# Performance work log

Measured on AMD Instinct MI355X. Metric: run time of the kernel, lower is better.

Reference implementation:

```python
import jax, jax.numpy as jnp
import numpy as np

B, T, D = 8, 8192, 768
H, HD = 12, 64            # heads, head_dim
Q_STRIDE = 4              # flattened 2x2 q pooling
WINDOW = 64               # flattened mask-unit size after pooling
SCALE = HD ** -0.5


def setup_inputs() -> dict:
    key = jax.random.key(0)
    ks = jax.random.split(key, 5)
    return {
        "embeddings": jax.random.normal(ks[0], (B, T, D), jnp.float32),
        "qkv_w": jax.random.normal(ks[1], (3 * D, D), jnp.float32) * 0.02,
        "qkv_b": jax.random.normal(ks[2], (3 * D,), jnp.float32) * 0.02,
        "proj_w": jax.random.normal(ks[3], (D, D), jnp.float32) * 0.02,
        "proj_b": jax.random.normal(ks[4], (D,), jnp.float32) * 0.02,
    }


def reference(embeddings, qkv_w, qkv_b, proj_w, proj_b):
    b, t, _ = embeddings.shape
    nw = t // (Q_STRIDE * WINDOW)          # number of mask-unit windows
    seq = t // nw                           # tokens per window (pre q-pool)
    # qkv: [b, t, 3D] -> [b, seq, nw, 3, H, HD] (windows are interleaved along tokens)
    qkv = (embeddings @ qkv_w.T + qkv_b).reshape(b, seq, nw, 3, H, HD)
    qkv = jnp.transpose(qkv, (3, 0, 4, 2, 1, 5))  # [3, b, H, nw, seq, HD]
    q, k, v = qkv[0], qkv[1], qkv[2]
    # q max-pool over stride groups (interleaved split of seq)
    q = q.reshape(b, H, nw, Q_STRIDE, seq // Q_STRIDE, HD).max(axis=3)
    attn = jax.nn.softmax(
        jnp.einsum("bhwqd,bhwkd->bhwqk", q * SCALE, k), axis=-1
    )  # [b, H, nw, q_len, seq]
    out = jnp.einsum("bhwqk,bhwkd->bhwqd", attn, v)  # [b, H, nw, q_len, HD]
    out = jnp.transpose(out, (0, 3, 2, 1, 4)).reshape(b, -1, H * HD)
    out = out @ proj_w.T + proj_b
    return out, attn
```

## Files before the change

kernel.cpp:

```cpp
#include <hip/hip_runtime.h>
#include <hip/hip_bf16.h>


typedef float  f32x4  __attribute__((ext_vector_type(4)));
typedef __bf16 bf16x8 __attribute__((ext_vector_type(8)));

__device__ __forceinline__ unsigned short f2bf(float f) {
  unsigned int u = __float_as_uint(f);
  u += 0x7fffu + ((u >> 16) & 1u);
  return (unsigned short)(u >> 16);
}
__device__ __forceinline__ float bf2f(unsigned short b) {
  return __uint_as_float(((unsigned int)b) << 16);
}

#define GLOAD_LDS16(gptr, lptr) __builtin_amdgcn_global_load_lds( \
    (const __attribute__((address_space(1))) void*)(gptr),        \
    (__attribute__((address_space(3))) void*)(lptr), 16, 0, 0)

__global__ void cvt_bf16(const float* __restrict__ src,
                         unsigned short* __restrict__ dst, int n4) {
  int i = blockIdx.x * blockDim.x + threadIdx.x;
  const int stride = gridDim.x * blockDim.x;
  for (; i < n4; i += stride) {
    const float4 v = ((const float4*)src)[i];
    ushort4 o;
    o.x = f2bf(v.x); o.y = f2bf(v.y); o.z = f2bf(v.z); o.w = f2bf(v.w);
    ((ushort4*)dst)[i] = o;
  }
}

template <int OUT_BF16>
__global__ __launch_bounds__(512, 2) void gemm256p(
    const unsigned short* __restrict__ A, const unsigned short* __restrict__ B,
    const float* __restrict__ bias, void* __restrict__ Cout,
    int M, int N, int K) {
  extern __shared__ char lds[];

  const int tid  = threadIdx.x;
  const int lane = tid & 63;
  const int wid  = tid >> 6;
  const int g16  = (lane >> 4) & 3;
  const int l15  = lane & 15;
  const int wm   = wid >> 2;
  const int wn   = wid & 3;

  const size_t bm = (size_t)blockIdx.x << 8;
  const int NT = K >> 6;
  const int NB = N >> 8;
  const int TT = NB * NT;

  const int srow = tid >> 2;
  const int csel = (((tid & 3) ^ ((tid >> 3) & 3)) << 3);
  const int ldst = wid * 1024;
  const unsigned short* pA0 = A + (bm + srow) * (size_t)K + csel;
  const unsigned short* pA1 = pA0 + (size_t)128 * K;
  const unsigned short* pB0 = B + (size_t)srow * K + csel;
  const unsigned short* pB1 = pB0 + (size_t)128 * K;

#define STAGE_A(koff, regbase)                                          \
  do {                                                                  \
    GLOAD_LDS16(pA0 + (koff), lds + (regbase) + ldst);                  \
    GLOAD_LDS16(pA1 + (koff), lds + (regbase) + 8192 + ldst);           \
  } while (0)
#define STAGE_B(boff, regbase)                                          \
  do {                                                                  \
    GLOAD_LDS16(pB0 + (boff), lds + (regbase) + ldst);                  \
    GLOAD_LDS16(pB1 + (boff), lds + (regbase) + 8192 + ldst);           \
  } while (0)

  const int s16  = ((g16 ^ ((l15 >> 1) & 3)) << 4);
  const int offA = (wm * 128 + l15) * 64 + s16;
  const int offB = (wn * 64 + l15) * 64 + s16;

  f32x4 acc[8][4];
  const f32x4 zero4 = {0.f, 0.f, 0.f, 0.f};
#pragma unroll
  for (int i = 0; i < 8; ++i)
#pragma unroll
    for (int j = 0; j < 4; ++j) acc[i][j] = zero4;

#define READ_A(par, kk, rh)                                              \
  { const char* rb = lds + (par) * 32768 + (kk) * 16384 + offA + (rh) * 4096; \
    af[0] = *(const bf16x8*)(rb);                                        \
    af[1] = *(const bf16x8*)(rb + 1024);                                 \
    af[2] = *(const bf16x8*)(rb + 2048);                                 \
    af[3] = *(const bf16x8*)(rb + 3072); }
#define READ_B(par, kk)                                                  \
  { const char* rb = lds + 65536 + (par) * 32768 + (kk) * 16384 + offB;  \
    bfv[0] = *(const bf16x8*)(rb);                                       \
    bfv[1] = *(const bf16x8*)(rb + 1024);                                \
    bfv[2] = *(const bf16x8*)(rb + 2048);                                \
    bfv[3] = *(const bf16x8*)(rb + 3072); }
#define MFMA16(rh)                                                       \
  _Pragma("unroll") for (int q = 0; q < 4; ++q)                          \
  _Pragma("unroll") for (int c = 0; c < 4; ++c)                          \
    acc[(rh) * 4 + q][c] = __builtin_amdgcn_mfma_f32_16x16x32_bf16(      \
        af[q], bfv[c], acc[(rh) * 4 + q][c], 0, 0, 0);
#define BAR() __builtin_amdgcn_s_barrier()
#define VMCNT8() asm volatile("s_waitcnt vmcnt(8)" ::: "memory")

  int    kk  = 0;
  int    bnC = 0;
  int    k1  = 64;
  int    k2  = 128;
  size_t rB1 = 0;
  size_t rB2 = 0;

  STAGE_A(0, 0);
  STAGE_B(0, 65536);
  STAGE_A(32, 16384);
  STAGE_B(32, 65536 + 16384);
  STAGE_A(64, 32768);
  STAGE_B(64, 65536 + 32768);
  VMCNT8();
  BAR();

  for (int s = 0; s < TT; ++s) {
    const int par  = s & 1;
    const int parn = par ^ 1;
    bf16x8 af[4], bfv[4];

    READ_A(par, 0, 0); READ_B(par, 0);
    STAGE_A(k1 + 32, parn * 32768 + 16384);
    BAR();
    __builtin_amdgcn_s_setprio(1); MFMA16(0); __builtin_amdgcn_s_setprio(0);
    BAR();

    READ_A(par, 0, 1);
    STAGE_B(rB1 + k1 + 32, 65536 + parn * 32768 + 16384);
    VMCNT8();
    BAR();
    __builtin_amdgcn_s_setprio(1); MFMA16(1); __builtin_amdgcn_s_setprio(0);
    BAR();

    READ_A(par, 1, 0); READ_B(par, 1);
    STAGE_A(k2, par * 32768);
    BAR();
    __builtin_amdgcn_s_setprio(1); MFMA16(0); __builtin_amdgcn_s_setprio(0);
    BAR();

    READ_A(par, 1, 1);
    STAGE_B(rB2 + k2, 65536 + par * 32768);
    VMCNT8();
    BAR();
    __builtin_amdgcn_s_setprio(1); MFMA16(1); __builtin_amdgcn_s_setprio(0);
    BAR();

    if (kk == NT - 1) {
#pragma unroll
      for (int ai = 0; ai < 8; ++ai) {
        const size_t row0 =
            bm + wm * 128 + (ai >> 2) * 64 + (ai & 3) * 16 + g16 * 4;
#pragma unroll
        for (int c = 0; c < 4; ++c) {
          const int col = bnC + wn * 64 + c * 16 + l15;
          const float bv = bias[col];
#pragma unroll
          for (int r = 0; r < 4; ++r) {
            const float v = acc[ai][c][r] + bv;
            const size_t idx = (row0 + r) * (size_t)N + col;
            if (OUT_BF16) ((unsigned short*)Cout)[idx] = f2bf(v);
            else          ((float*)Cout)[idx] = v;
          }
          acc[ai][c] = zero4;
        }
      }
      bnC += 256;
      kk = 0;
    } else {
      ++kk;
    }

    k1 = k2; rB1 = rB2;
    if (s + 3 < TT) {
      k2 += 64;
      if (k2 == K) { k2 = 0; rB2 += (size_t)256 * K; }
    }
  }
#undef STAGE_A
#undef STAGE_B
#undef READ_A
#undef READ_B
#undef MFMA16
#undef BAR
#undef VMCNT8
}

template <int OUT_BF16>
__global__ __launch_bounds__(256) void gemm_bt(
    const unsigned short* __restrict__ A, const unsigned short* __restrict__ B,
    const float* __restrict__ bias, void* __restrict__ Cout,
    int M, int N, int K) {
  __shared__ unsigned short As[128 * 64];
  __shared__ unsigned short Bs[128 * 64];

  const int tid  = threadIdx.x;
  const int lane = tid & 63;
  const int wid  = tid >> 6;
  const int g16  = lane >> 4;
  const int l15  = lane & 15;
  const int bm = blockIdx.x * 128;
  const int bn = blockIdx.y * 128;
  const int wr = (wid >> 1) * 64;
  const int wc = (wid & 1) * 64;

  const f32x4 zero4 = {0.f, 0.f, 0.f, 0.f};
  f32x4 acc[4][4];
#pragma unroll
  for (int m = 0; m < 4; ++m)
#pragma unroll
    for (int n = 0; n < 4; ++n) acc[m][n] = zero4;

  const int flatBase = tid * 16;

  for (int kt = 0; kt < K; kt += 64) {
#pragma unroll
    for (int c = 0; c < 4; ++c) {
      const int flat = c * 4096 + flatBase;
      const int row  = flat >> 7;
      const int cole = (flat & 127) >> 1;
      const unsigned short* ga = A + (size_t)(bm + row) * K + kt + cole;
      const unsigned short* gb = B + (size_t)(bn + row) * K + kt + cole;
      GLOAD_LDS16(ga, (char*)As + c * 4096 + wid * 1024);
      GLOAD_LDS16(gb, (char*)Bs + c * 4096 + wid * 1024);
    }
    __syncthreads();
#pragma unroll
    for (int kk = 0; kk < 2; ++kk) {
      bf16x8 af[4], bfv[4];
#pragma unroll
      for (int m = 0; m < 4; ++m)
        af[m] = *(const bf16x8*)((const char*)As +
                 ((wr + m * 16 + l15) * 64 + kk * 32 + g16 * 8) * 2);
#pragma unroll
      for (int n = 0; n < 4; ++n)
        bfv[n] = *(const bf16x8*)((const char*)Bs +
                 ((wc + n * 16 + l15) * 64 + kk * 32 + g16 * 8) * 2);
#pragma unroll
      for (int m = 0; m < 4; ++m)
#pragma unroll
        for (int n = 0; n < 4; ++n)
          acc[m][n] = __builtin_amdgcn_mfma_f32_16x16x32_bf16(af[m], bfv[n],
                                                              acc[m][n], 0, 0, 0);
    }
    __syncthreads();
  }

#pragma unroll
  for (int n = 0; n < 4; ++n) {
    const int col = bn + wc + n * 16 + l15;
    const float bv = bias[col];
#pragma unroll
    for (int m = 0; m < 4; ++m) {
      const int rowb = bm + wr + m * 16 + g16 * 4;
#pragma unroll
      for (int r = 0; r < 4; ++r) {
        const float v = acc[m][n][r] + bv;
        const size_t idx = (size_t)(rowb + r) * N + col;
        if (OUT_BF16) ((unsigned short*)Cout)[idx] = f2bf(v);
        else          ((float*)Cout)[idx] = v;
      }
    }
  }
}

__global__ __launch_bounds__(256) void attn_kernel(
    const unsigned short* __restrict__ qkv,
    float* __restrict__ attn_out,
    unsigned short* __restrict__ Xws) {
  __shared__ unsigned short smem[32768];
  char* KP = (char*)smem;
  char* VT = (char*)(smem + 16384);

  const int tid  = threadIdx.x;
  const int lane = tid & 63;
  const int wid  = tid >> 6;
  const int g16  = lane >> 4;
  const int l15  = lane & 15;

  const int bid = blockIdx.x;
  const int w = bid & 31;
  const int h = (bid >> 5) % 12;
  const int b = bid / 384;

  {
    const int s0 = tid >> 3;
    const int part = tid & 7;
#pragma unroll
    for (int p = 0; p < 8; ++p) {
      const int s = s0 + p * 32;
      const size_t gbase =
          ((size_t)b * 8192 + (size_t)s * 32 + w) * 2304 + h * 64 + part * 8;
      int4 kv = *(const int4*)(qkv + gbase + 768);
      *(int4*)(KP + ((s * 128 + part * 16) ^ ((s & 7) << 4))) = kv;
      int4 vv = *(const int4*)(qkv + gbase + 1536);
      const unsigned short* pv = (const unsigned short*)&vv;
#pragma unroll
      for (int j = 0; j < 8; ++j) {
        const int d = part * 8 + j;
        *(unsigned short*)(VT + ((d * 512 + s * 2) ^ ((d & 7) << 4))) = pv[j];
      }
    }
  }

  union BU { unsigned short u[8]; bf16x8 v; };
  BU aq0, aq1;
  {
    const int qrow = wid * 16 + l15;
    float q0[8], q1[8];
#pragma unroll
    for (int j = 0; j < 8; ++j) { q0[j] = -1e30f; q1[j] = -1e30f; }
#pragma unroll
    for (int g = 0; g < 4; ++g) {
      const size_t gbase =
          ((size_t)b * 8192 + (size_t)(g * 64 + qrow) * 32 + w) * 2304 +
          h * 64 + g16 * 8;
      int4 a = *(const int4*)(qkv + gbase);
      int4 c = *(const int4*)(qkv + gbase + 32);
      const unsigned short* pa = (const unsigned short*)&a;
      const unsigned short* pc = (const unsigned short*)&c;
#pragma unroll
      for (int j = 0; j < 8; ++j) {
        q0[j] = fmaxf(q0[j], bf2f(pa[j]));
        q1[j] = fmaxf(q1[j], bf2f(pc[j]));
      }
    }
#pragma unroll
    for (int j = 0; j < 8; ++j) {
      aq0.u[j] = (unsigned short)(__float_as_uint(q0[j]) >> 16);
      aq1.u[j] = (unsigned short)(__float_as_uint(q1[j]) >> 16);
    }
  }

  __syncthreads();

  f32x4 sacc[16];
  const f32x4 zero4 = {0.f, 0.f, 0.f, 0.f};
#pragma unroll
  for (int t = 0; t < 16; ++t) sacc[t] = zero4;
#pragma unroll
  for (int t = 0; t < 16; ++t) {
    const int srow = t * 16 + l15;
    bf16x8 bk0 = *(const bf16x8*)(KP + ((srow * 128 + 0  + g16 * 16) ^ ((srow & 7) << 4)));
    bf16x8 bk1 = *(const bf16x8*)(KP + ((srow * 128 + 64 + g16 * 16) ^ ((srow & 7) << 4)));
    sacc[t] = __builtin_amdgcn_mfma_f32_16x16x32_bf16(aq0.v, bk0, sacc[t], 0, 0, 0);
    sacc[t] = __builtin_amdgcn_mfma_f32_16x16x32_bf16(aq1.v, bk1, sacc[t], 0, 0, 0);
  }

  float inv_[4];
#pragma unroll
  for (int r = 0; r < 4; ++r) {
    float m = -1e30f;
#pragma unroll
    for (int t = 0; t < 16; ++t) { sacc[t][r] *= 0.125f; m = fmaxf(m, sacc[t][r]); }
#pragma unroll
    for (int off = 1; off < 16; off <<= 1) m = fmaxf(m, __shfl_xor(m, off, 64));
    float ssum = 0.f;
#pragma unroll
    for (int t = 0; t < 16; ++t) {
      float e = expf(sacc[t][r] - m);
      sacc[t][r] = e;
      ssum += e;
    }
#pragma unroll
    for (int off = 1; off < 16; off <<= 1) ssum += __shfl_xor(ssum, off, 64);
    inv_[r] = 1.f / ssum;
  }

  {
    float* ab = attn_out + ((size_t)bid * 64 + wid * 16) * 256;
#pragma unroll
    for (int t = 0; t < 16; ++t)
#pragma unroll
      for (int r = 0; r < 4; ++r) {
        const float p = sacc[t][r] * inv_[r];
        sacc[t][r] = p;
        ab[(size_t)(g16 * 4 + r) * 256 + t * 16 + l15] = p;
      }
  }

  __syncthreads();

  {
    char* PW = KP + wid * 8192;
#pragma unroll
    for (int t = 0; t < 16; ++t)
#pragma unroll
      for (int r = 0; r < 4; ++r) {
        const int row = g16 * 4 + r;
        *(unsigned short*)(PW + ((row * 512 + (t * 16 + l15) * 2) ^ ((row & 7) << 4))) =
            f2bf(sacc[t][r]);
      }
  }

  f32x4 oacc[4];
#pragma unroll
  for (int n = 0; n < 4; ++n) oacc[n] = zero4;
  {
    const char* PR = KP + wid * 8192;
#pragma unroll
    for (int kc = 0; kc < 8; ++kc) {
      bf16x8 pa = *(const bf16x8*)(PR + ((l15 * 512 + kc * 64 + g16 * 16) ^ ((l15 & 7) << 4)));
#pragma unroll
      for (int n = 0; n < 4; ++n) {
        const int d = n * 16 + l15;
        bf16x8 vv = *(const bf16x8*)(VT + ((d * 512 + kc * 64 + g16 * 16) ^ ((d & 7) << 4)));
        oacc[n] = __builtin_amdgcn_mfma_f32_16x16x32_bf16(pa, vv, oacc[n], 0, 0, 0);
      }
    }
  }

#pragma unroll
  for (int n = 0; n < 4; ++n)
#pragma unroll
    for (int r = 0; r < 4; ++r) {
      const int qi = wid * 16 + g16 * 4 + r;
      Xws[((size_t)b * 2048 + qi * 32 + w) * 768 + h * 64 + n * 16 + l15] =
          f2bf(oacc[n][r]);
    }
}

extern "C" void kernel_launch(void* const* d_in, const int* in_sizes, int n_in,
                              void* d_out, int out_size, void* d_ws, size_t ws_size,
                              hipStream_t stream) {
  const float* emb    = (const float*)d_in[0];
  const float* qkv_w  = (const float*)d_in[1];
  const float* qkv_b  = (const float*)d_in[2];
  const float* proj_w = (const float*)d_in[3];
  const float* proj_b = (const float*)d_in[4];
  float* out = (float*)d_out;

  char* ws = (char*)d_ws;
  unsigned short* embB   = (unsigned short*)(ws);
  unsigned short* wqkvB  = (unsigned short*)(ws + 100663296);
  unsigned short* wprojB = (unsigned short*)(ws + 104202240);
  unsigned short* qkvB   = (unsigned short*)(ws + 105381888);
  unsigned short* Xws    = (unsigned short*)(ws + 407371776);

  cvt_bf16<<<4096, 256, 0, stream>>>(emb, embB, 50331648 / 4);
  cvt_bf16<<<1728, 256, 0, stream>>>(qkv_w, wqkvB, 1769472 / 4);
  cvt_bf16<<<576, 256, 0, stream>>>(proj_w, wprojB, 589824 / 4);

  hipFuncSetAttribute(reinterpret_cast<const void*>(&gemm256p<1>),
                      hipFuncAttributeMaxDynamicSharedMemorySize, 131072);
  gemm256p<1><<<256, 512, 131072, stream>>>(embB, wqkvB, qkv_b, qkvB,
                                            65536, 2304, 768);

  attn_kernel<<<3072, 256, 0, stream>>>(qkvB, out + 12582912, Xws);

  gemm_bt<0><<<dim3(128, 6), 256, 0, stream>>>(Xws, wprojB, proj_b, out,
                                               16384, 768, 768);
}
```

Baseline: 489.5 us.

## Double-buffer LDS fragment registers to prefetch next MFMA operands

```diff
diff --git a/kernel.cpp b/kernel.cpp
--- a/kernel.cpp
+++ b/kernel.cpp
@@ -80,25 +80,27 @@
 #pragma unroll
     for (int j = 0; j < 4; ++j) acc[i][j] = zero4;
 
-#define READ_A(par, kk, rh)                                              \
+  bf16x8 aA[4], aB[4], bA[4], bB[4];
+
+#define READ_A_TO(dst, par, kk, rh)                                      \
   { const char* rb = lds + (par) * 32768 + (kk) * 16384 + offA + (rh) * 4096; \
-    af[0] = *(const bf16x8*)(rb);                                        \
-    af[1] = *(const bf16x8*)(rb + 1024);                                 \
-    af[2] = *(const bf16x8*)(rb + 2048);                                 \
-    af[3] = *(const bf16x8*)(rb + 3072); }
-#define READ_B(par, kk)                                                  \
+    dst[0] = *(const bf16x8*)(rb);                                       \
+    dst[1] = *(const bf16x8*)(rb + 1024);                                \
+    dst[2] = *(const bf16x8*)(rb + 2048);                                \
+    dst[3] = *(const bf16x8*)(rb + 3072); }
+#define READ_B_TO(dst, par, kk)                                          \
   { const char* rb = lds + 65536 + (par) * 32768 + (kk) * 16384 + offB;  \
-    bfv[0] = *(const bf16x8*)(rb);                                       \
-    bfv[1] = *(const bf16x8*)(rb + 1024);                                \
-    bfv[2] = *(const bf16x8*)(rb + 2048);                                \
-    bfv[3] = *(const bf16x8*)(rb + 3072); }
-#define MFMA16(rh)                                                       \
+    dst[0] = *(const bf16x8*)(rb);                                       \
+    dst[1] = *(const bf16x8*)(rb + 1024);                                \
+    dst[2] = *(const bf16x8*)(rb + 2048);                                \
+    dst[3] = *(const bf16x8*)(rb + 3072); }
+#define MFMA16(av, bv, rh)                                               \
   _Pragma("unroll") for (int q = 0; q < 4; ++q)                          \
   _Pragma("unroll") for (int c = 0; c < 4; ++c)                          \
     acc[(rh) * 4 + q][c] = __builtin_amdgcn_mfma_f32_16x16x32_bf16(      \
-        af[q], bfv[c], acc[(rh) * 4 + q][c], 0, 0, 0);
+        av[q], bv[c], acc[(rh) * 4 + q][c], 0, 0, 0);
 #define BAR() __builtin_amdgcn_s_barrier()
-#define VMCNT8() asm volatile("s_waitcnt vmcnt(8)" ::: "memory")
+#define VMCNT6() asm volatile("s_waitcnt vmcnt(6)" ::: "memory")
 
   int    kk  = 0;
   int    bnC = 0;
@@ -113,38 +115,41 @@
   STAGE_B(32, 65536 + 16384);
   STAGE_A(64, 32768);
   STAGE_B(64, 65536 + 32768);
-  VMCNT8();
+  asm volatile("s_waitcnt vmcnt(8)" ::: "memory");
   BAR();
+  READ_A_TO(aA, 0, 0, 0);
+  READ_B_TO(bA, 0, 0);
 
   for (int s = 0; s < TT; ++s) {
     const int par  = s & 1;
     const int parn = par ^ 1;
-    bf16x8 af[4], bfv[4];
-
-    READ_A(par, 0, 0); READ_B(par, 0);
+
+    READ_A_TO(aB, par, 0, 1);
     STAGE_A(k1 + 32, parn * 32768 + 16384);
-    BAR();
-    __builtin_amdgcn_s_setprio(1); MFMA16(0); __builtin_amdgcn_s_setprio(0);
-    BAR();
-
-    READ_A(par, 0, 1);
+    VMCNT6();
+    BAR();
+    __builtin_amdgcn_s_setprio(1); MFMA16(aA, bA, 0); __builtin_amdgcn_s_setprio(0);
+    BAR();
+
+    READ_A_TO(aA, par, 1, 0);
+    READ_B_TO(bB, par, 1);
     STAGE_B(rB1 + k1 + 32, 65536 + parn * 32768 + 16384);
-    VMCNT8();
-    BAR();
-    __builtin_amdgcn_s_setprio(1); MFMA16(1); __builtin_amdgcn_s_setprio(0);
-    BAR();
-
-    READ_A(par, 1, 0); READ_B(par, 1);
+    BAR();
+    __builtin_amdgcn_s_setprio(1); MFMA16(aB, bA, 1); __builtin_amdgcn_s_setprio(0);
+    BAR();
+
+    READ_A_TO(aB, par, 1, 1);
     STAGE_A(k2, par * 32768);
-    BAR();
-    __builtin_amdgcn_s_setprio(1); MFMA16(0); __builtin_amdgcn_s_setprio(0);
-    BAR();
-
-    READ_A(par, 1, 1);
+    VMCNT6();
+    BAR();
+    __builtin_amdgcn_s_setprio(1); MFMA16(aA, bB, 0); __builtin_amdgcn_s_setprio(0);
+    BAR();
+
+    READ_A_TO(aA, parn, 0, 0);
+    READ_B_TO(bA, parn, 0);
     STAGE_B(rB2 + k2, 65536 + par * 32768);
-    VMCNT8();
-    BAR();
-    __builtin_amdgcn_s_setprio(1); MFMA16(1); __builtin_amdgcn_s_setprio(0);
+    BAR();
+    __builtin_amdgcn_s_setprio(1); MFMA16(aB, bB, 1); __builtin_amdgcn_s_setprio(0);
     BAR();
 
     if (kk == NT - 1) {
@@ -180,11 +185,11 @@
   }
 #undef STAGE_A
 #undef STAGE_B
-#undef READ_A
-#undef READ_B
+#undef READ_A_TO
+#undef READ_B_TO
 #undef MFMA16
 #undef BAR
-#undef VMCNT8
+#undef VMCNT6
 }
 
 template <int OUT_BF16>
```

Result: no change. 487.5 us (-0.4%).

## Swizzle GEMM LDS tiles and vectorize V transpose stores in attention

Applied to the files above, without the earlier changes.

```diff
diff --git a/kernel.cpp b/kernel.cpp
--- a/kernel.cpp
+++ b/kernel.cpp
@@ -213,17 +213,19 @@
     for (int n = 0; n < 4; ++n) acc[m][n] = zero4;
 
   const int flatBase = tid * 16;
+  const int rsw = l15 & 3;
 
   for (int kt = 0; kt < K; kt += 64) {
 #pragma unroll
     for (int c = 0; c < 4; ++c) {
       const int flat = c * 4096 + flatBase;
       const int row  = flat >> 7;
-      const int cole = (flat & 127) >> 1;
+      const int slot = (flat >> 4) & 7;
+      const int cole = (((slot) ^ (row & 3)) << 3);
       const unsigned short* ga = A + (size_t)(bm + row) * K + kt + cole;
       const unsigned short* gb = B + (size_t)(bn + row) * K + kt + cole;
-      GLOAD_LDS16(ga, (char*)As + c * 4096 + wid * 1024);
-      GLOAD_LDS16(gb, (char*)Bs + c * 4096 + wid * 1024);
+      GLOAD_LDS16(ga, (char*)As + c * 4096 + wid * 1024 + lane * 16);
+      GLOAD_LDS16(gb, (char*)Bs + c * 4096 + wid * 1024 + lane * 16);
     }
     __syncthreads();
 #pragma unroll
@@ -232,11 +234,11 @@
 #pragma unroll
       for (int m = 0; m < 4; ++m)
         af[m] = *(const bf16x8*)((const char*)As +
-                 ((wr + m * 16 + l15) * 64 + kk * 32 + g16 * 8) * 2);
+                 (wr + m * 16 + l15) * 128 + (((kk * 4 + g16) ^ rsw) << 4));
 #pragma unroll
       for (int n = 0; n < 4; ++n)
         bfv[n] = *(const bf16x8*)((const char*)Bs +
-                 ((wc + n * 16 + l15) * 64 + kk * 32 + g16 * 8) * 2);
+                 (wc + n * 16 + l15) * 128 + (((kk * 4 + g16) ^ rsw) << 4));
 #pragma unroll
       for (int m = 0; m < 4; ++m)
 #pragma unroll
@@ -284,23 +286,43 @@
   const int h = (bid >> 5) % 12;
   const int b = bid / 384;
 
-  {
-    const int s0 = tid >> 3;
-    const int part = tid & 7;
-#pragma unroll
-    for (int p = 0; p < 8; ++p) {
-      const int s = s0 + p * 32;
-      const size_t gbase =
-          ((size_t)b * 8192 + (size_t)s * 32 + w) * 2304 + h * 64 + part * 8;
-      int4 kv = *(const int4*)(qkv + gbase + 768);
-      *(int4*)(KP + ((s * 128 + part * 16) ^ ((s & 7) << 4))) = kv;
-      int4 vv = *(const int4*)(qkv + gbase + 1536);
-      const unsigned short* pv = (const unsigned short*)&vv;
-#pragma unroll
-      for (int j = 0; j < 8; ++j) {
-        const int d = part * 8 + j;
-        *(unsigned short*)(VT + ((d * 512 + s * 2) ^ ((d & 7) << 4))) = pv[j];
-      }
+  const int s0 = tid >> 3;
+  const int part = tid & 7;
+
+#pragma unroll
+  for (int p = 0; p < 8; ++p) {
+    const int s = s0 + p * 32;
+    const size_t gbase =
+        ((size_t)b * 8192 + (size_t)s * 32 + w) * 2304 + h * 64 + part * 8;
+    int4 kv = *(const int4*)(qkv + gbase + 768);
+    *(int4*)(KP + ((s * 128 + part * 16) ^ ((s & 7) << 4))) = kv;
+  }
+
+#pragma unroll
+  for (int p = 0; p < 2; ++p) {
+    const int s = s0 * 4 + p * 128;
+    const size_t gb0 =
+        ((size_t)b * 8192 + (size_t)s * 32 + w) * 2304 + 1536 + h * 64 + part * 8;
+    int4 x0 = *(const int4*)(qkv + gb0);
+    int4 x1 = *(const int4*)(qkv + gb0 + 73728);
+    int4 x2 = *(const int4*)(qkv + gb0 + 147456);
+    int4 x3 = *(const int4*)(qkv + gb0 + 221184);
+    const unsigned int* u0 = (const unsigned int*)&x0;
+    const unsigned int* u1 = (const unsigned int*)&x1;
+    const unsigned int* u2 = (const unsigned int*)&x2;
+    const unsigned int* u3 = (const unsigned int*)&x3;
+#pragma unroll
+    for (int k = 0; k < 4; ++k) {
+      const unsigned int lo01 = (u0[k] & 0xffffu) | (u1[k] << 16);
+      const unsigned int lo23 = (u2[k] & 0xffffu) | (u3[k] << 16);
+      const unsigned int hi01 = (u0[k] >> 16) | (u1[k] & 0xffff0000u);
+      const unsigned int hi23 = (u2[k] >> 16) | (u3[k] & 0xffff0000u);
+      const int dlo = part * 8 + 2 * k;
+      const int dhi = dlo + 1;
+      uint2 vlo; vlo.x = lo01; vlo.y = lo23;
+      uint2 vhi; vhi.x = hi01; vhi.y = hi23;
+      *(uint2*)(VT + ((dlo * 512 + s * 2) ^ ((dlo & 7) << 4))) = vlo;
+      *(uint2*)(VT + ((dhi * 512 + s * 2) ^ ((dhi & 7) << 4))) = vhi;
     }
   }
 
```

After: 482.4 us. About the same (-1.5%).
